# Kernel optimization log

Hardware: AMD Instinct MI355X
Metric: run time of the kernel (lower is better)

## Reference

```python
import jax, jax.numpy as jnp
import numpy as np

D_MODEL = 128
NHEAD = 8
NLAYERS = 6
LAYER_NAMES = ['self', 'cross', 'self', 'cross', 'self', 'cross']
TEMPERATURE = 5.0
EPS = 1e-6


def _pos_encoding(x):
    # Sinusoidal 1D position encoding along the width axis. x: [N, H, W, C]
    C, W = x.shape[-1], x.shape[2]
    pos = jnp.arange(W, dtype=x.dtype)[:, None]                      # [W,1]
    div = jnp.exp(jnp.arange(0, C, 2, dtype=x.dtype) * (-np.log(10000.0) / C))
    pe = jnp.zeros((W, C), x.dtype)
    pe = pe.at[:, 0::2].set(jnp.sin(pos * div))
    pe = pe.at[:, 1::2].set(jnp.cos(pos * div))
    return x + pe[None, None]                                        # broadcast over N,H


def _linear_attention(q, k, v):
    # q,k,v: [N, H, W, nhead, dim]; kernelized linear attention along W
    Q = jax.nn.elu(q) + 1.0
    K = jax.nn.elu(k) + 1.0
    v_len = v.shape[2]
    V = v / v_len
    KV = jnp.einsum('nhsed,nhsev->nhedv', K, V)                      # [N,H,e,d,d]
    Z = 1.0 / (jnp.einsum('nhled,nhed->nhle', Q, K.sum(axis=2)) + EPS)
    return jnp.einsum('nhled,nhedv,nhle->nhlev', Q, KV, Z) * v_len


def _layer_norm(x, g, b):
    m = x.mean(-1, keepdims=True)
    v = jnp.mean((x - m) ** 2, -1, keepdims=True)
    return (x - m) / jnp.sqrt(v + 1e-5) * g + b


def _encoder_layer(x, source, Wq, Wk, Wv, Wm, W1, W2, g1, b1, g2, b2):
    x = _pos_encoding(x)
    source = _pos_encoding(source)
    bs, h, w, c = x.shape
    e, d = NHEAD, c // NHEAD
    q = (x @ Wq).reshape(bs, h, w, e, d)
    k = (source @ Wk).reshape(bs, h, w, e, d)
    v = (source @ Wv).reshape(bs, h, w, e, d)
    msg = _linear_attention(q, k, v).reshape(bs, h, w, c) @ Wm
    msg = _layer_norm(msg, g1, b1)
    msg = jnp.concatenate([x, msg], axis=-1)                         # [N,H,W,2C]
    msg = jax.nn.relu(msg @ W1) @ W2
    msg = _layer_norm(msg, g2, b2)
    return x + msg


def _forward(feat0, feat1, Wq, Wk, Wv, Wm, W1, W2, g1, b1, g2, b2):
    feat0 = feat0.transpose(0, 2, 3, 1)                              # [N,H,W,C]
    feat1 = feat1.transpose(0, 2, 3, 1)
    for i, name in enumerate(LAYER_NAMES):
        p = (Wq[i], Wk[i], Wv[i], Wm[i], W1[i], W2[i], g1[i], b1[i], g2[i], b2[i])
        if name == 'self':
            feat0 = _encoder_layer(feat0, feat0, *p)
            feat1 = _encoder_layer(feat1, feat1, *p)
        else:  # cross: sequential update (feat1 sees updated feat0), as in torch source
            feat0 = _encoder_layer(feat0, feat1, *p)
            feat1 = _encoder_layer(feat1, feat0, *p)
    w = feat0.shape[2]
    attn_mask = jnp.where(jnp.triu(jnp.ones((w, w), bool), 1), -jnp.inf, 0.0)
    attn_mask = attn_mask[None, None].astype(feat0.dtype)
    scale = feat0.shape[-1] ** 0.5
    sim = jnp.einsum('ntwc,ntlc->ntwl', feat0 / scale, feat1 / scale) / TEMPERATURE
    return sim + attn_mask


def setup_inputs() -> dict:
    key = jax.random.key(0)
    ks = jax.random.split(key, 12)
    N, C, H, W = 2, D_MODEL, 64, 640
    L, D = NLAYERS, D_MODEL
    s = 1.0 / np.sqrt(D)
    s2 = 1.0 / np.sqrt(2 * D)
    return {
        'feat0': jax.random.normal(ks[0], (N, C, H, W), jnp.float32),
        'feat1': jax.random.normal(ks[1], (N, C, H, W), jnp.float32),
        'Wq': jax.random.normal(ks[2], (L, D, D), jnp.float32) * s,
        'Wk': jax.random.normal(ks[3], (L, D, D), jnp.float32) * s,
        'Wv': jax.random.normal(ks[4], (L, D, D), jnp.float32) * s,
        'Wm': jax.random.normal(ks[5], (L, D, D), jnp.float32) * s,
        'W1': jax.random.normal(ks[6], (L, 2 * D, 2 * D), jnp.float32) * s2,
        'W2': jax.random.normal(ks[7], (L, 2 * D, D), jnp.float32) * s2,
        'g1': jnp.ones((L, D), jnp.float32),
        'b1': jnp.zeros((L, D), jnp.float32),
        'g2': jnp.ones((L, D), jnp.float32),
        'b2': jnp.zeros((L, D), jnp.float32),
    }


def reference(feat0, feat1, Wq, Wk, Wv, Wm, W1, W2, g1, b1, g2, b2):
    return _forward(feat0, feat1, Wq, Wk, Wv, Wm, W1, W2, g1, b1, g2, b2)
```

## Files before the change

### kernel.cpp

```cpp
#include <hip/hip_runtime.h>
#include <cmath>
#include <math.h>

#define TOK 81920
#define WDIM 640

typedef __attribute__((ext_vector_type(8))) short short8v;
typedef __attribute__((ext_vector_type(4))) short short4v;
typedef __attribute__((ext_vector_type(4))) float f32x4;

__device__ __forceinline__ short f2bf(float f) {
  __bf16 h = (__bf16)f;
  short s;
  __builtin_memcpy(&s, &h, 2);
  return s;
}
__device__ __forceinline__ float bf2f(short s) {
  union { unsigned u; float f; } x; x.u = ((unsigned)(unsigned short)s) << 16;
  return x.f;
}

__global__ __launch_bounds__(256) void pe_kernel(float* __restrict__ pe) {
  int id = blockIdx.x * 256 + threadIdx.x;
  if (id >= WDIM * 128) return;
  int w = id >> 7;
  int c = id & 127;
  float i2 = (float)(c & 126);
  float freq = expf(i2 * -0.071955784156063941f);
  float ang = (float)w * freq;
  pe[id] = (c & 1) ? cosf(ang) : sinf(ang);
}

__global__ __launch_bounds__(256) void tr_kernel(const float* __restrict__ in0,
                                                 const float* __restrict__ in1,
                                                 short* __restrict__ x0,
                                                 short* __restrict__ x1) {
  __shared__ float t[32][33];
  int w0 = blockIdx.x * 32;
  int c0 = blockIdx.y * 32;
  int z = blockIdx.z;
  int feat = z >> 7;
  int nh = z & 127;
  int n = nh >> 6, h = nh & 63;
  const float* in = feat ? in1 : in0;
  short* out = feat ? x1 : x0;
  int tx = threadIdx.x & 31, ty = threadIdx.x >> 5;
  const float* ip = in + ((n * 128 + c0) * 64 + h) * 640 + w0;
#pragma unroll
  for (int i = 0; i < 32; i += 8)
    t[ty + i][tx] = ip[(ty + i) * (64 * 640) + tx];
  __syncthreads();
  short* op = out + ((size_t)(n * 64 + h) * 640 + w0) * 128 + c0;
#pragma unroll
  for (int i = 0; i < 32; i += 8)
    op[(size_t)(ty + i) * 128 + tx] = f2bf(t[tx][ty + i]);
}

__global__ __launch_bounds__(256) void wprep_kernel(
    const float* __restrict__ Wq, const float* __restrict__ Wk,
    const float* __restrict__ Wv, const float* __restrict__ Wm,
    const float* __restrict__ W1, const float* __restrict__ W2,
    short* __restrict__ BT) {
  int id = blockIdx.x * 256 + threadIdx.x;
  if (id >= 6 * 163840) return;
  int layer = id / 163840;
  int r = id % 163840;
  float v;
  if (r < 65536) {
    int seg = r >> 14;
    int rr = r & 16383;
    int n = rr >> 7, k = rr & 127;
    const float* W = seg == 0 ? Wq : seg == 1 ? Wk : seg == 2 ? Wv : Wm;
    v = W[layer * 16384 + k * 128 + n];
  } else if (r < 131072) {
    int rr = r - 65536;
    int n = rr >> 8, k = rr & 255;
    v = W1[layer * 65536 + k * 256 + n];
  } else {
    int rr = r - 131072;
    int n = rr >> 8, k = rr & 255;
    v = W2[layer * 32768 + k * 128 + n];
  }
  BT[id] = f2bf(v);
}

__device__ __forceinline__ void load_af(const short* __restrict__ A,
                                        const float* __restrict__ pe,
                                        int bm, int wr, int l15, int lk,
                                        short8v af[4][4]) {
  const int wbase = bm % WDIM;
#pragma unroll
  for (int mf = 0; mf < 4; ++mf) {
    const int rl = wr * 64 + mf * 16 + l15;
    const short* ar = A + (size_t)(bm + rl) * 128;
    const float* pr = pe + (size_t)(wbase + rl) * 128;
#pragma unroll
    for (int ks = 0; ks < 4; ++ks) {
      const int kloc = ks * 32 + lk * 8;
      short8v xa = *(const short8v*)(ar + kloc);
      f32x4 p0 = *(const f32x4*)(pr + kloc);
      f32x4 p1 = *(const f32x4*)(pr + kloc + 4);
      short8v o;
      o[0] = f2bf(bf2f(xa[0]) + p0[0]); o[1] = f2bf(bf2f(xa[1]) + p0[1]);
      o[2] = f2bf(bf2f(xa[2]) + p0[2]); o[3] = f2bf(bf2f(xa[3]) + p0[3]);
      o[4] = f2bf(bf2f(xa[4]) + p1[0]); o[5] = f2bf(bf2f(xa[5]) + p1[1]);
      o[6] = f2bf(bf2f(xa[6]) + p1[2]); o[7] = f2bf(bf2f(xa[7]) + p1[3]);
      af[ks][mf] = o;
    }
  }
}

__device__ __forceinline__ void proj_pass_T(const short8v af[4][4],
                                            const short* __restrict__ WT,
                                            int wr, int wc, int l15, int lk,
                                            short (*tS)[136]) {
  f32x4 acc[4][4] = {};
#pragma unroll
  for (int ks = 0; ks < 4; ++ks) {
    const int kloc = ks * 32 + lk * 8;
    short8v bfr[4];
#pragma unroll
    for (int nf = 0; nf < 4; ++nf)
      bfr[nf] = *(const short8v*)&WT[(size_t)(wc * 64 + nf * 16 + l15) * 128 + kloc];
#pragma unroll
    for (int mf = 0; mf < 4; ++mf)
#pragma unroll
      for (int nf = 0; nf < 4; ++nf)
        acc[mf][nf] = __builtin_amdgcn_mfma_f32_16x16x32_bf16(
            bfr[nf], af[ks][mf], acc[mf][nf], 0, 0, 0);
  }
#pragma unroll
  for (int mf = 0; mf < 4; ++mf)
#pragma unroll
    for (int nf = 0; nf < 4; ++nf) {
      short4v p;
      p[0] = f2bf(acc[mf][nf][0]); p[1] = f2bf(acc[mf][nf][1]);
      p[2] = f2bf(acc[mf][nf][2]); p[3] = f2bf(acc[mf][nf][3]);
      *(short4v*)&tS[wr * 64 + mf * 16 + l15][wc * 64 + nf * 16 + lk * 4] = p;
    }
}

__device__ __forceinline__ void tile_out(const short (*tS)[136], int bm, int tid,
                                         short* __restrict__ out) {
#pragma unroll
  for (int it = 0; it < 8; ++it) {
    int u = it * 256 + tid;
    int row = u >> 4, seg = u & 15;
    *(short8v*)&out[(size_t)(bm + row) * 128 + seg * 8] =
        *(const short8v*)&tS[row][seg * 8];
  }
}

__global__ __launch_bounds__(256) void qkv_self_kernel(
    const short* __restrict__ x0, const short* __restrict__ x1,
    const float* __restrict__ pe,
    const short* __restrict__ wqT, const short* __restrict__ wkT,
    const short* __restrict__ wvT,
    short* q0, short* k0, short* v0, short* q1, short* k1, short* v1) {
  __shared__ short tS[128][136];
  const int tid = threadIdx.x, lane = tid & 63, wid = tid >> 6;
  const int wr = wid >> 1, wc = wid & 1;
  const int bm = blockIdx.x * 128;
  const int l15 = lane & 15, lk = lane >> 4;
  const int z = blockIdx.z;
  const short* A = z ? x1 : x0;
  short8v af[4][4];
  load_af(A, pe, bm, wr, l15, lk, af);
  proj_pass_T(af, wqT, wr, wc, l15, lk, tS);
  __syncthreads();
  tile_out(tS, bm, tid, z ? q1 : q0);
  __syncthreads();
  proj_pass_T(af, wkT, wr, wc, l15, lk, tS);
  __syncthreads();
  tile_out(tS, bm, tid, z ? k1 : k0);
  __syncthreads();
  proj_pass_T(af, wvT, wr, wc, l15, lk, tS);
  __syncthreads();
  tile_out(tS, bm, tid, z ? v1 : v0);
}

__global__ __launch_bounds__(256) void qkv_cross_kernel(
    const short* __restrict__ xq, const short* __restrict__ xs,
    const float* __restrict__ pe,
    const short* __restrict__ wqT, const short* __restrict__ wkT,
    const short* __restrict__ wvT,
    short* qb, short* kb, short* vb) {
  __shared__ short tS[128][136];
  const int tid = threadIdx.x, lane = tid & 63, wid = tid >> 6;
  const int wr = wid >> 1, wc = wid & 1;
  const int bm = blockIdx.x * 128;
  const int l15 = lane & 15, lk = lane >> 4;
  short8v af[4][4];
  if (blockIdx.y == 0) {
    load_af(xq, pe, bm, wr, l15, lk, af);
    proj_pass_T(af, wqT, wr, wc, l15, lk, tS);
    __syncthreads();
    tile_out(tS, bm, tid, qb);
  } else {
    load_af(xs, pe, bm, wr, l15, lk, af);
    proj_pass_T(af, wkT, wr, wc, l15, lk, tS);
    __syncthreads();
    tile_out(tS, bm, tid, kb);
    __syncthreads();
    proj_pass_T(af, wvT, wr, wc, l15, lk, tS);
    __syncthreads();
    tile_out(tS, bm, tid, vb);
  }
}

template <int NSC>
__global__ __launch_bounds__(256) void kv_kernel(
    const short* __restrict__ k0, const short* __restrict__ v0,
    const short* __restrict__ k1, const short* __restrict__ v1,
    float* __restrict__ kvp) {
  const int bid = blockIdx.x;
  const int sc = bid % NSC;
  const int e = bid / NSC;
  const int strip = sc / 5, chunk = sc % 5;
  const short* kb = (strip >= 128) ? k1 : k0;
  const short* vb = (strip >= 128) ? v1 : v0;
  const int nh = strip & 127;
  const size_t base = (size_t)nh * (640 * 128) + (size_t)chunk * (128 * 128) + e * 16;
  __shared__ float Ks[128][16];
  __shared__ float Vs[128][16];
  const int tid = threadIdx.x;
  const int srow = tid >> 1, shalf = (tid & 1) * 8;
  short8v k8 = *(const short8v*)&kb[base + (size_t)srow * 128 + shalf];
  short8v v8 = *(const short8v*)&vb[base + (size_t)srow * 128 + shalf];
#pragma unroll
  for (int j = 0; j < 8; ++j) {
    float kr = bf2f(k8[j]);
    Ks[srow][shalf + j] = kr > 0.f ? kr + 1.f : __expf(kr);
    Vs[srow][shalf + j] = bf2f(v8[j]);
  }
  __syncthreads();
  const int d = tid >> 4, vv = tid & 15;
  float kv = 0.f, ks = 0.f;
#pragma unroll 8
  for (int sl = 0; sl < 128; ++sl) {
    float kk = Ks[sl][d];
    kv = fmaf(kk, Vs[sl][vv], kv);
    ks += kk;
  }
  float* out = kvp + ((size_t)(strip * 8 + e) * 5 + chunk) * 272;
  out[d * 16 + vv] = kv;
  if (vv == 0) out[256 + d] = ks;
}

template <int DUAL>
__global__ __launch_bounds__(256) void apply_wm_kernel(
    short* q0, short* q1, const float* __restrict__ kvp,
    const short* __restrict__ wmT,
    const float* __restrict__ g, const float* __restrict__ b) {
  const int bid = blockIdx.x;
  const int strip = bid / 10, lc = bid % 10;
  __shared__ float KV8[8][16][17];
  __shared__ float KS8[8][16];
  __shared__ short oS[64][136];
  const int tid = threadIdx.x;
  for (int idx = tid; idx < 8 * 272; idx += 256) {
    int e = idx / 272, r = idx - e * 272;
    const float* p = kvp + ((size_t)(strip * 8 + e) * 5) * 272 + r;
    float s = ((p[0] + p[272]) + (p[544] + p[816])) + p[1088];
    if (r < 256) KV8[e][r >> 4][r & 15] = s;
    else         KS8[e][r - 256] = s;
  }
  __syncthreads();
  short* qb = (DUAL && strip >= 128) ? q1 : q0;
  const int nh = strip & 127;
  const int lrow = tid >> 2;
  const int row = lc * 64 + lrow;
  const int cb = (tid & 3) * 32;
  short* qp = qb + (size_t)nh * (640 * 128) + (size_t)row * 128 + cb;
  short8v qv0 = *(const short8v*)(qp);
  short8v qv1 = *(const short8v*)(qp + 8);
  short8v qv2 = *(const short8v*)(qp + 16);
  short8v qv3 = *(const short8v*)(qp + 24);
  float qe[32];
#pragma unroll
  for (int j = 0; j < 8; ++j) {
    float a = bf2f(qv0[j]); qe[j]      = a > 0.f ? a + 1.f : __expf(a);
    float c1 = bf2f(qv1[j]); qe[8 + j]  = c1 > 0.f ? c1 + 1.f : __expf(c1);
    float c2 = bf2f(qv2[j]); qe[16 + j] = c2 > 0.f ? c2 + 1.f : __expf(c2);
    float c3 = bf2f(qv3[j]); qe[24 + j] = c3 > 0.f ? c3 + 1.f : __expf(c3);
  }
  short res[32];
#pragma unroll
  for (int h = 0; h < 2; ++h) {
    const int e = (cb >> 4) + h;
    const float* Q = qe + h * 16;
    float dz = 0.f;
#pragma unroll
    for (int dd = 0; dd < 16; ++dd) dz = fmaf(Q[dd], KS8[e][dd], dz);
    const float zi = 1.f / (dz + 1e-6f);
#pragma unroll
    for (int vv = 0; vv < 16; ++vv) {
      float o = 0.f;
#pragma unroll
      for (int dd = 0; dd < 16; ++dd) o = fmaf(Q[dd], KV8[e][dd][vv], o);
      res[h * 16 + vv] = f2bf(o * zi);
    }
  }
  short8v w0, w1, w2, w3;
#pragma unroll
  for (int j = 0; j < 8; ++j) {
    w0[j] = res[j]; w1[j] = res[8 + j]; w2[j] = res[16 + j]; w3[j] = res[24 + j];
  }
  *(short8v*)&oS[lrow][cb]      = w0;
  *(short8v*)&oS[lrow][cb + 8]  = w1;
  *(short8v*)&oS[lrow][cb + 16] = w2;
  *(short8v*)&oS[lrow][cb + 24] = w3;
  __syncthreads();
  const int lane = tid & 63, wv = tid >> 6;
  const int l15 = lane & 15, lk = lane >> 4;
  f32x4 acc[8] = {};
#pragma unroll
  for (int ks = 0; ks < 4; ++ks) {
    const int kloc = ks * 32 + lk * 8;
    short8v afr = *(const short8v*)&oS[wv * 16 + l15][kloc];
    short8v bfr[8];
#pragma unroll
    for (int nf = 0; nf < 8; ++nf)
      bfr[nf] = *(const short8v*)&wmT[(size_t)(nf * 16 + l15) * 128 + kloc];
#pragma unroll
    for (int nf = 0; nf < 8; ++nf)
      acc[nf] = __builtin_amdgcn_mfma_f32_16x16x32_bf16(bfr[nf], afr, acc[nf], 0, 0, 0);
  }
  float s = 0.f, qq = 0.f;
#pragma unroll
  for (int nf = 0; nf < 8; ++nf)
#pragma unroll
    for (int r = 0; r < 4; ++r) {
      s += acc[nf][r];
      qq = fmaf(acc[nf][r], acc[nf][r], qq);
    }
  s += __shfl_xor(s, 16);  qq += __shfl_xor(qq, 16);
  s += __shfl_xor(s, 32);  qq += __shfl_xor(qq, 32);
  float mean = s * (1.f / 128.f);
  float var = qq * (1.f / 128.f) - mean * mean;
  float rstd = rsqrtf(var + 1e-5f);
#pragma unroll
  for (int nf = 0; nf < 8; ++nf) {
    f32x4 g4 = *(const f32x4*)&g[nf * 16 + lk * 4];
    f32x4 b4 = *(const f32x4*)&b[nf * 16 + lk * 4];
    short4v p;
#pragma unroll
    for (int r = 0; r < 4; ++r)
      p[r] = f2bf((acc[nf][r] - mean) * rstd * g4[r] + b4[r]);
    *(short4v*)&oS[wv * 16 + l15][nf * 16 + lk * 4] = p;
  }
  __syncthreads();
  short* mp = qb + (size_t)nh * (640 * 128) + (size_t)(lc * 64) * 128;
#pragma unroll
  for (int it = 0; it < 4; ++it) {
    int u = it * 256 + tid;
    int rw = u >> 4, seg = u & 15;
    *(short8v*)&mp[(size_t)rw * 128 + seg * 8] = *(const short8v*)&oS[rw][seg * 8];
  }
}

__global__ __launch_bounds__(256) void w1_kernel(
    const short* __restrict__ xA, const short* __restrict__ xB,
    const short* __restrict__ mA, const short* __restrict__ mB,
    const float* __restrict__ pe, const short* __restrict__ w1T,
    short* h0A, short* h1A, short* h0B, short* h1B) {
  __shared__ short tS[128][136];
  const int z = blockIdx.z;
  const short* x = z ? xB : xA;
  const short* m = z ? mB : mA;
  short* h0 = z ? h0B : h0A;
  short* h1 = z ? h1B : h1A;
  const int tid = threadIdx.x, lane = tid & 63, wid = tid >> 6;
  const int wr = wid >> 1, wc = wid & 1;
  const int bm = blockIdx.x * 128;
  const int l15 = lane & 15, lk = lane >> 4;
  const int wbase = bm % WDIM;
  for (int p = 0; p < 2; ++p) {
    f32x4 acc[4][4] = {};
#pragma unroll
    for (int ks = 0; ks < 8; ++ks) {
      const int kloc = ks * 32 + lk * 8;
      short8v bfr[4], afr[4];
#pragma unroll
      for (int nf = 0; nf < 4; ++nf)
        bfr[nf] = *(const short8v*)&w1T[(size_t)(p * 128 + wc * 64 + nf * 16 + l15) * 256 + kloc];
      if (ks < 4) {
#pragma unroll
        for (int mf = 0; mf < 4; ++mf) {
          const int rl = wr * 64 + mf * 16 + l15;
          short8v xa = *(const short8v*)(x + (size_t)(bm + rl) * 128 + kloc);
          const float* pr = pe + (size_t)(wbase + rl) * 128 + kloc;
          f32x4 p0 = *(const f32x4*)pr;
          f32x4 p1 = *(const f32x4*)(pr + 4);
          short8v ov;
          ov[0] = f2bf(bf2f(xa[0]) + p0[0]); ov[1] = f2bf(bf2f(xa[1]) + p0[1]);
          ov[2] = f2bf(bf2f(xa[2]) + p0[2]); ov[3] = f2bf(bf2f(xa[3]) + p0[3]);
          ov[4] = f2bf(bf2f(xa[4]) + p1[0]); ov[5] = f2bf(bf2f(xa[5]) + p1[1]);
          ov[6] = f2bf(bf2f(xa[6]) + p1[2]); ov[7] = f2bf(bf2f(xa[7]) + p1[3]);
          afr[mf] = ov;
        }
      } else {
#pragma unroll
        for (int mf = 0; mf < 4; ++mf)
          afr[mf] = *(const short8v*)&m[(size_t)(bm + wr * 64 + mf * 16 + l15) * 128 + kloc - 128];
      }
#pragma unroll
      for (int mf = 0; mf < 4; ++mf)
#pragma unroll
        for (int nf = 0; nf < 4; ++nf)
          acc[mf][nf] = __builtin_amdgcn_mfma_f32_16x16x32_bf16(
              bfr[nf], afr[mf], acc[mf][nf], 0, 0, 0);
    }
#pragma unroll
    for (int mf = 0; mf < 4; ++mf)
#pragma unroll
      for (int nf = 0; nf < 4; ++nf) {
        short4v pk;
#pragma unroll
        for (int r = 0; r < 4; ++r)
          pk[r] = f2bf(fmaxf(acc[mf][nf][r], 0.f));
        *(short4v*)&tS[wr * 64 + mf * 16 + l15][wc * 64 + nf * 16 + lk * 4] = pk;
      }
    __syncthreads();
    tile_out(tS, bm, tid, p ? h1 : h0);
    __syncthreads();
  }
}

__global__ __launch_bounds__(256) void w2_ln_kernel(
    const short* __restrict__ h0A, const short* __restrict__ h1A,
    const short* __restrict__ h0B, const short* __restrict__ h1B,
    const short* __restrict__ w2T, short* xA, short* xB,
    const float* __restrict__ pe, const float* __restrict__ g,
    const float* __restrict__ b) {
  __shared__ short tS[128][136];
  __shared__ float lds_s[2][128];
  __shared__ float lds_q[2][128];
  const int z = blockIdx.z;
  const short* h0 = z ? h0B : h0A;
  const short* h1 = z ? h1B : h1A;
  short* x = z ? xB : xA;
  const int tid = threadIdx.x, lane = tid & 63, wid = tid >> 6;
  const int wr = wid >> 1, wc = wid & 1;
  const int bm = blockIdx.x * 128;
  const int l15 = lane & 15, lk = lane >> 4;
  const int wbase = bm % WDIM;
  f32x4 acc[4][4] = {};
#pragma unroll
  for (int ks = 0; ks < 8; ++ks) {
    const int kloc = ks * 32 + lk * 8;
    const short* hp = (ks < 4) ? h0 : h1;
    const int kl = (ks < 4) ? kloc : kloc - 128;
    short8v bfr[4], afr[4];
#pragma unroll
    for (int nf = 0; nf < 4; ++nf)
      bfr[nf] = *(const short8v*)&w2T[(size_t)(wc * 64 + nf * 16 + l15) * 256 + kloc];
#pragma unroll
    for (int mf = 0; mf < 4; ++mf)
      afr[mf] = *(const short8v*)&hp[(size_t)(bm + wr * 64 + mf * 16 + l15) * 128 + kl];
#pragma unroll
    for (int mf = 0; mf < 4; ++mf)
#pragma unroll
      for (int nf = 0; nf < 4; ++nf)
        acc[mf][nf] = __builtin_amdgcn_mfma_f32_16x16x32_bf16(
            bfr[nf], afr[mf], acc[mf][nf], 0, 0, 0);
  }
#pragma unroll
  for (int mf = 0; mf < 4; ++mf) {
    float s = 0.f, qq = 0.f;
#pragma unroll
    for (int nf = 0; nf < 4; ++nf)
#pragma unroll
      for (int r = 0; r < 4; ++r) {
        s += acc[mf][nf][r];
        qq = fmaf(acc[mf][nf][r], acc[mf][nf][r], qq);
      }
    s += __shfl_xor(s, 16);  qq += __shfl_xor(qq, 16);
    s += __shfl_xor(s, 32);  qq += __shfl_xor(qq, 32);
    if (lk == 0) {
      int rl = wr * 64 + mf * 16 + l15;
      lds_s[wc][rl] = s;
      lds_q[wc][rl] = qq;
    }
  }
  __syncthreads();
#pragma unroll
  for (int mf = 0; mf < 4; ++mf) {
    int rl = wr * 64 + mf * 16 + l15;
    float mean = (lds_s[0][rl] + lds_s[1][rl]) * (1.f / 128.f);
    float var = (lds_q[0][rl] + lds_q[1][rl]) * (1.f / 128.f) - mean * mean;
    float rstd = rsqrtf(var + 1e-5f);
#pragma unroll
    for (int nf = 0; nf < 4; ++nf) {
      f32x4 g4 = *(const f32x4*)&g[wc * 64 + nf * 16 + lk * 4];
      f32x4 b4 = *(const f32x4*)&b[wc * 64 + nf * 16 + lk * 4];
      short4v pk;
#pragma unroll
      for (int r = 0; r < 4; ++r)
        pk[r] = f2bf((acc[mf][nf][r] - mean) * rstd * g4[r] + b4[r]);
      *(short4v*)&tS[rl][wc * 64 + nf * 16 + lk * 4] = pk;
    }
  }
  __syncthreads();
#pragma unroll
  for (int it = 0; it < 8; ++it) {
    int u = it * 256 + tid;
    int row = u >> 4, seg = u & 15;
    size_t xi = (size_t)(bm + row) * 128 + seg * 8;
    short8v xv8 = *(const short8v*)&x[xi];
    short8v t8 = *(const short8v*)&tS[row][seg * 8];
    const float* pr = pe + (size_t)(wbase + row) * 128 + seg * 8;
    f32x4 p0 = *(const f32x4*)pr;
    f32x4 p1 = *(const f32x4*)(pr + 4);
    short8v o8;
    o8[0] = f2bf(bf2f(xv8[0]) + p0[0] + bf2f(t8[0]));
    o8[1] = f2bf(bf2f(xv8[1]) + p0[1] + bf2f(t8[1]));
    o8[2] = f2bf(bf2f(xv8[2]) + p0[2] + bf2f(t8[2]));
    o8[3] = f2bf(bf2f(xv8[3]) + p0[3] + bf2f(t8[3]));
    o8[4] = f2bf(bf2f(xv8[4]) + p1[0] + bf2f(t8[4]));
    o8[5] = f2bf(bf2f(xv8[5]) + p1[1] + bf2f(t8[5]));
    o8[6] = f2bf(bf2f(xv8[6]) + p1[2] + bf2f(t8[6]));
    o8[7] = f2bf(bf2f(xv8[7]) + p1[3] + bf2f(t8[7]));
    *(short8v*)&x[xi] = o8;
  }
}

__global__ __launch_bounds__(256) void sim_mfma(const short* __restrict__ f0,
                                                const short* __restrict__ f1,
                                                float* __restrict__ out) {
  const int fid = (blockIdx.z * 5 + blockIdx.y) * 5 + blockIdx.x;
  const int c8 = fid & 7, kk_ = fid >> 3;
  const int nt = c8 * 16 + kk_ / 25;
  const int r2 = kk_ % 25;
  const int bw = (r2 % 5) * 128;
  const int bl = (r2 / 5) * 128;
  const int tid = threadIdx.x;
  if (bl > bw) {
    f32x4 m4 = {-1e30f, -1e30f, -1e30f, -1e30f};
#pragma unroll
    for (int it = 0; it < 16; ++it) {
      int u = it * 256 + tid;
      int row = u >> 5, c4 = u & 31;
      *(f32x4*)&out[((size_t)nt * 640 + bw + row) * 640 + bl + c4 * 4] = m4;
    }
    return;
  }
  const int lane = tid & 63;
  const int wid = tid >> 6;
  const int wr = wid >> 1, wc = wid & 1;
  const short* __restrict__ A = f0 + (size_t)nt * 640 * 128;
  const short* __restrict__ B = f1 + (size_t)nt * 640 * 128;
  const int l15 = lane & 15;
  const int lk = lane >> 4;
  f32x4 acc[4][4] = {};
#pragma unroll
  for (int ks = 0; ks < 4; ++ks) {
    const int kloc = ks * 32 + lk * 8;
    short8v afr[4], bfr[4];
#pragma unroll
    for (int mf = 0; mf < 4; ++mf)
      afr[mf] = *(const short8v*)&A[(size_t)(bw + wr * 64 + mf * 16 + l15) * 128 + kloc];
#pragma unroll
    for (int nf = 0; nf < 4; ++nf)
      bfr[nf] = *(const short8v*)&B[(size_t)(bl + wc * 64 + nf * 16 + l15) * 128 + kloc];
#pragma unroll
    for (int mf = 0; mf < 4; ++mf)
#pragma unroll
      for (int nf = 0; nf < 4; ++nf)
        acc[mf][nf] = __builtin_amdgcn_mfma_f32_16x16x32_bf16(
            afr[mf], bfr[nf], acc[mf][nf], 0, 0, 0);
  }
#pragma unroll
  for (int mf = 0; mf < 4; ++mf)
#pragma unroll
    for (int nf = 0; nf < 4; ++nf) {
      const int l = bl + wc * 64 + nf * 16 + l15;
#pragma unroll
      for (int r = 0; r < 4; ++r) {
        const int w = bw + wr * 64 + mf * 16 + lk * 4 + r;
        float v = acc[mf][nf][r] * (1.f / 640.f);
        if (l > w) v = -1e30f;
        out[((size_t)nt * 640 + w) * 640 + l] = v;
      }
    }
}

extern "C" void kernel_launch(void* const* d_in, const int* in_sizes, int n_in,
                              void* d_out, int out_size, void* d_ws, size_t ws_size,
                              hipStream_t stream) {
  (void)in_sizes; (void)n_in; (void)out_size; (void)ws_size;
  const float* feat0 = (const float*)d_in[0];
  const float* feat1 = (const float*)d_in[1];
  const float* Wq = (const float*)d_in[2];
  const float* Wk = (const float*)d_in[3];
  const float* Wv = (const float*)d_in[4];
  const float* Wm = (const float*)d_in[5];
  const float* W1 = (const float*)d_in[6];
  const float* W2 = (const float*)d_in[7];
  const float* g1 = (const float*)d_in[8];
  const float* b1 = (const float*)d_in[9];
  const float* g2 = (const float*)d_in[10];
  const float* b2 = (const float*)d_in[11];

  float* wsf = (float*)d_ws;
  const size_t U = (size_t)TOK * 128;
  float* pe = wsf;
  short* x0 = (short*)(wsf + 81920);
  short* x1 = x0 + U;
  short* q0 = x1 + U;
  short* k0 = q0 + U;
  short* v0 = k0 + U;
  short* q1 = v0 + U;
  short* k1 = q1 + U;
  short* v1 = k1 + U;
  short* bt = v1 + U;
  float* kvp = (float*)(bt + 983040);

  dim3 blk(256);
  pe_kernel<<<dim3(320), blk, 0, stream>>>(pe);
  tr_kernel<<<dim3(20, 4, 256), blk, 0, stream>>>(feat0, feat1, x0, x1);
  wprep_kernel<<<dim3((6 * 163840 + 255) / 256), blk, 0, stream>>>(
      Wq, Wk, Wv, Wm, W1, W2, bt);

  const int NB = TOK / 128;
  for (int i = 0; i < 6; ++i) {
    const short* bt_i = bt + (size_t)i * 163840;
    const short* wqT = bt_i;
    const short* wkT = bt_i + 16384;
    const short* wvT = bt_i + 32768;
    const short* wmT = bt_i + 49152;
    const short* w1T = bt_i + 65536;
    const short* w2T = bt_i + 131072;
    const float* g1_i = g1 + i * 128;
    const float* b1_i = b1 + i * 128;
    const float* g2_i = g2 + i * 128;
    const float* b2_i = b2 + i * 128;
    if ((i & 1) == 0) {
      qkv_self_kernel<<<dim3(NB, 1, 2), blk, 0, stream>>>(
          x0, x1, pe, wqT, wkT, wvT, q0, k0, v0, q1, k1, v1);
      kv_kernel<1280><<<dim3(8 * 1280), blk, 0, stream>>>(k0, v0, k1, v1, kvp);
      apply_wm_kernel<1><<<dim3(2560), blk, 0, stream>>>(q0, q1, kvp, wmT, g1_i, b1_i);
      w1_kernel<<<dim3(NB, 1, 2), blk, 0, stream>>>(
          x0, x1, q0, q1, pe, w1T, k0, v0, k1, v1);
      w2_ln_kernel<<<dim3(NB, 1, 2), blk, 0, stream>>>(
          k0, v0, k1, v1, w2T, x0, x1, pe, g2_i, b2_i);
    } else {
      qkv_cross_kernel<<<dim3(NB, 2), blk, 0, stream>>>(
          x0, x1, pe, wqT, wkT, wvT, q0, k0, v0);
      kv_kernel<640><<<dim3(8 * 640), blk, 0, stream>>>(k0, v0, k0, v0, kvp);
      apply_wm_kernel<0><<<dim3(1280), blk, 0, stream>>>(q0, q0, kvp, wmT, g1_i, b1_i);
      w1_kernel<<<dim3(NB, 1, 1), blk, 0, stream>>>(
          x0, x0, q0, q0, pe, w1T, k0, v0, k0, v0);
      w2_ln_kernel<<<dim3(NB, 1, 1), blk, 0, stream>>>(
          k0, v0, k0, v0, w2T, x0, x0, pe, g2_i, b2_i);

      qkv_cross_kernel<<<dim3(NB, 2), blk, 0, stream>>>(
          x1, x0, pe, wqT, wkT, wvT, q0, k0, v0);
      kv_kernel<640><<<dim3(8 * 640), blk, 0, stream>>>(k0, v0, k0, v0, kvp);
      apply_wm_kernel<0><<<dim3(1280), blk, 0, stream>>>(q0, q0, kvp, wmT, g1_i, b1_i);
      w1_kernel<<<dim3(NB, 1, 1), blk, 0, stream>>>(
          x1, x1, q0, q0, pe, w1T, k0, v0, k0, v0);
      w2_ln_kernel<<<dim3(NB, 1, 1), blk, 0, stream>>>(
          k0, v0, k0, v0, w2T, x1, x1, pe, g2_i, b2_i);
    }
  }
  sim_mfma<<<dim3(5, 5, 128), blk, 0, stream>>>(x0, x1, (float*)d_out);
}
```

Baseline: 2.381 ms.

## Shrink projection and FFN GEMM tiles to 64 rows with 4 column-split waves

The QKV, W1 and W2+LayerNorm kernels now process 64-row tiles instead of 128, with each of the four waves covering all 64 rows and a 32-column slice rather than a 2x2 wave grid. This doubles the block count and halves accumulator registers and shared memory, aiming at better occupancy and load balance across CUs. The LayerNorm row reduction now combines four wave partials, and the LDS row pitch changes to 140. In exchange, each wave repeats the activation loads and the positional-encoding add, so per-block reuse of A fragments goes down.

```diff
diff --git a/kernel.cpp b/kernel.cpp
--- a/kernel.cpp
+++ b/kernel.cpp
@@ -84,14 +84,15 @@
   BT[id] = f2bf(v);
 }
 
-__device__ __forceinline__ void load_af(const short* __restrict__ A,
-                                        const float* __restrict__ pe,
-                                        int bm, int wr, int l15, int lk,
-                                        short8v af[4][4]) {
+
+__device__ __forceinline__ void load_af64(const short* __restrict__ A,
+                                          const float* __restrict__ pe,
+                                          int bm, int l15, int lk,
+                                          short8v af[4][4]) {
   const int wbase = bm % WDIM;
 #pragma unroll
   for (int mf = 0; mf < 4; ++mf) {
-    const int rl = wr * 64 + mf * 16 + l15;
+    const int rl = mf * 16 + l15;
     const short* ar = A + (size_t)(bm + rl) * 128;
     const float* pr = pe + (size_t)(wbase + rl) * 128;
 #pragma unroll
@@ -110,40 +111,40 @@
   }
 }
 
-__device__ __forceinline__ void proj_pass_T(const short8v af[4][4],
+__device__ __forceinline__ void proj_pass64(const short8v af[4][4],
                                             const short* __restrict__ WT,
-                                            int wr, int wc, int l15, int lk,
-                                            short (*tS)[136]) {
-  f32x4 acc[4][4] = {};
+                                            int wq, int l15, int lk,
+                                            short (*tS)[140]) {
+  f32x4 acc[4][2] = {};
 #pragma unroll
   for (int ks = 0; ks < 4; ++ks) {
     const int kloc = ks * 32 + lk * 8;
-    short8v bfr[4];
-#pragma unroll
-    for (int nf = 0; nf < 4; ++nf)
-      bfr[nf] = *(const short8v*)&WT[(size_t)(wc * 64 + nf * 16 + l15) * 128 + kloc];
+    short8v bfr[2];
+#pragma unroll
+    for (int nf = 0; nf < 2; ++nf)
+      bfr[nf] = *(const short8v*)&WT[(size_t)(wq * 32 + nf * 16 + l15) * 128 + kloc];
 #pragma unroll
     for (int mf = 0; mf < 4; ++mf)
 #pragma unroll
-      for (int nf = 0; nf < 4; ++nf)
+      for (int nf = 0; nf < 2; ++nf)
         acc[mf][nf] = __builtin_amdgcn_mfma_f32_16x16x32_bf16(
             bfr[nf], af[ks][mf], acc[mf][nf], 0, 0, 0);
   }
 #pragma unroll
   for (int mf = 0; mf < 4; ++mf)
 #pragma unroll
-    for (int nf = 0; nf < 4; ++nf) {
+    for (int nf = 0; nf < 2; ++nf) {
       short4v p;
       p[0] = f2bf(acc[mf][nf][0]); p[1] = f2bf(acc[mf][nf][1]);
       p[2] = f2bf(acc[mf][nf][2]); p[3] = f2bf(acc[mf][nf][3]);
-      *(short4v*)&tS[wr * 64 + mf * 16 + l15][wc * 64 + nf * 16 + lk * 4] = p;
-    }
-}
-
-__device__ __forceinline__ void tile_out(const short (*tS)[136], int bm, int tid,
-                                         short* __restrict__ out) {
-#pragma unroll
-  for (int it = 0; it < 8; ++it) {
+      *(short4v*)&tS[mf * 16 + l15][wq * 32 + nf * 16 + lk * 4] = p;
+    }
+}
+
+__device__ __forceinline__ void tile_out64(const short (*tS)[140], int bm, int tid,
+                                           short* __restrict__ out) {
+#pragma unroll
+  for (int it = 0; it < 4; ++it) {
     int u = it * 256 + tid;
     int row = u >> 4, seg = u & 15;
     *(short8v*)&out[(size_t)(bm + row) * 128 + seg * 8] =
@@ -157,26 +158,25 @@
     const short* __restrict__ wqT, const short* __restrict__ wkT,
     const short* __restrict__ wvT,
     short* q0, short* k0, short* v0, short* q1, short* k1, short* v1) {
-  __shared__ short tS[128][136];
-  const int tid = threadIdx.x, lane = tid & 63, wid = tid >> 6;
-  const int wr = wid >> 1, wc = wid & 1;
-  const int bm = blockIdx.x * 128;
+  __shared__ short tS[64][140];
+  const int tid = threadIdx.x, lane = tid & 63, wq = tid >> 6;
+  const int bm = blockIdx.x * 64;
   const int l15 = lane & 15, lk = lane >> 4;
   const int z = blockIdx.z;
   const short* A = z ? x1 : x0;
   short8v af[4][4];
-  load_af(A, pe, bm, wr, l15, lk, af);
-  proj_pass_T(af, wqT, wr, wc, l15, lk, tS);
-  __syncthreads();
-  tile_out(tS, bm, tid, z ? q1 : q0);
-  __syncthreads();
-  proj_pass_T(af, wkT, wr, wc, l15, lk, tS);
-  __syncthreads();
-  tile_out(tS, bm, tid, z ? k1 : k0);
-  __syncthreads();
-  proj_pass_T(af, wvT, wr, wc, l15, lk, tS);
-  __syncthreads();
-  tile_out(tS, bm, tid, z ? v1 : v0);
+  load_af64(A, pe, bm, l15, lk, af);
+  proj_pass64(af, wqT, wq, l15, lk, tS);
+  __syncthreads();
+  tile_out64(tS, bm, tid, z ? q1 : q0);
+  __syncthreads();
+  proj_pass64(af, wkT, wq, l15, lk, tS);
+  __syncthreads();
+  tile_out64(tS, bm, tid, z ? k1 : k0);
+  __syncthreads();
+  proj_pass64(af, wvT, wq, l15, lk, tS);
+  __syncthreads();
+  tile_out64(tS, bm, tid, z ? v1 : v0);
 }
 
 __global__ __launch_bounds__(256) void qkv_cross_kernel(
@@ -185,26 +185,25 @@
     const short* __restrict__ wqT, const short* __restrict__ wkT,
     const short* __restrict__ wvT,
     short* qb, short* kb, short* vb) {
-  __shared__ short tS[128][136];
-  const int tid = threadIdx.x, lane = tid & 63, wid = tid >> 6;
-  const int wr = wid >> 1, wc = wid & 1;
-  const int bm = blockIdx.x * 128;
+  __shared__ short tS[64][140];
+  const int tid = threadIdx.x, lane = tid & 63, wq = tid >> 6;
+  const int bm = blockIdx.x * 64;
   const int l15 = lane & 15, lk = lane >> 4;
   short8v af[4][4];
   if (blockIdx.y == 0) {
-    load_af(xq, pe, bm, wr, l15, lk, af);
-    proj_pass_T(af, wqT, wr, wc, l15, lk, tS);
+    load_af64(xq, pe, bm, l15, lk, af);
+    proj_pass64(af, wqT, wq, l15, lk, tS);
     __syncthreads();
-    tile_out(tS, bm, tid, qb);
+    tile_out64(tS, bm, tid, qb);
   } else {
-    load_af(xs, pe, bm, wr, l15, lk, af);
-    proj_pass_T(af, wkT, wr, wc, l15, lk, tS);
+    load_af64(xs, pe, bm, l15, lk, af);
+    proj_pass64(af, wkT, wq, l15, lk, tS);
     __syncthreads();
-    tile_out(tS, bm, tid, kb);
+    tile_out64(tS, bm, tid, kb);
     __syncthreads();
-    proj_pass_T(af, wvT, wr, wc, l15, lk, tS);
+    proj_pass64(af, wvT, wq, l15, lk, tS);
     __syncthreads();
-    tile_out(tS, bm, tid, vb);
+    tile_out64(tS, bm, tid, vb);
   }
 }
 
@@ -364,30 +363,29 @@
     const short* __restrict__ mA, const short* __restrict__ mB,
     const float* __restrict__ pe, const short* __restrict__ w1T,
     short* h0A, short* h1A, short* h0B, short* h1B) {
-  __shared__ short tS[128][136];
+  __shared__ short tS[64][140];
   const int z = blockIdx.z;
   const short* x = z ? xB : xA;
   const short* m = z ? mB : mA;
   short* h0 = z ? h0B : h0A;
   short* h1 = z ? h1B : h1A;
-  const int tid = threadIdx.x, lane = tid & 63, wid = tid >> 6;
-  const int wr = wid >> 1, wc = wid & 1;
-  const int bm = blockIdx.x * 128;
+  const int tid = threadIdx.x, lane = tid & 63, wq = tid >> 6;
+  const int bm = blockIdx.x * 64;
   const int l15 = lane & 15, lk = lane >> 4;
   const int wbase = bm % WDIM;
   for (int p = 0; p < 2; ++p) {
-    f32x4 acc[4][4] = {};
+    f32x4 acc[4][2] = {};
 #pragma unroll
     for (int ks = 0; ks < 8; ++ks) {
       const int kloc = ks * 32 + lk * 8;
-      short8v bfr[4], afr[4];
-#pragma unroll
-      for (int nf = 0; nf < 4; ++nf)
-        bfr[nf] = *(const short8v*)&w1T[(size_t)(p * 128 + wc * 64 + nf * 16 + l15) * 256 + kloc];
+      short8v bfr[2], afr[4];
+#pragma unroll
+      for (int nf = 0; nf < 2; ++nf)
+        bfr[nf] = *(const short8v*)&w1T[(size_t)(p * 128 + wq * 32 + nf * 16 + l15) * 256 + kloc];
       if (ks < 4) {
 #pragma unroll
         for (int mf = 0; mf < 4; ++mf) {
-          const int rl = wr * 64 + mf * 16 + l15;
+          const int rl = mf * 16 + l15;
           short8v xa = *(const short8v*)(x + (size_t)(bm + rl) * 128 + kloc);
           const float* pr = pe + (size_t)(wbase + rl) * 128 + kloc;
           f32x4 p0 = *(const f32x4*)pr;
@@ -402,27 +400,27 @@
       } else {
 #pragma unroll
         for (int mf = 0; mf < 4; ++mf)
-          afr[mf] = *(const short8v*)&m[(size_t)(bm + wr * 64 + mf * 16 + l15) * 128 + kloc - 128];
+          afr[mf] = *(const short8v*)&m[(size_t)(bm + mf * 16 + l15) * 128 + kloc - 128];
       }
 #pragma unroll
       for (int mf = 0; mf < 4; ++mf)
 #pragma unroll
-        for (int nf = 0; nf < 4; ++nf)
+        for (int nf = 0; nf < 2; ++nf)
           acc[mf][nf] = __builtin_amdgcn_mfma_f32_16x16x32_bf16(
               bfr[nf], afr[mf], acc[mf][nf], 0, 0, 0);
     }
 #pragma unroll
     for (int mf = 0; mf < 4; ++mf)
 #pragma unroll
-      for (int nf = 0; nf < 4; ++nf) {
+      for (int nf = 0; nf < 2; ++nf) {
         short4v pk;
 #pragma unroll
         for (int r = 0; r < 4; ++r)
           pk[r] = f2bf(fmaxf(acc[mf][nf][r], 0.f));
-        *(short4v*)&tS[wr * 64 + mf * 16 + l15][wc * 64 + nf * 16 + lk * 4] = pk;
+        *(short4v*)&tS[mf * 16 + l15][wq * 32 + nf * 16 + lk * 4] = pk;
       }
     __syncthreads();
-    tile_out(tS, bm, tid, p ? h1 : h0);
+    tile_out64(tS, bm, tid, p ? h1 : h0);
     __syncthreads();
   }
 }
@@ -433,35 +431,34 @@
     const short* __restrict__ w2T, short* xA, short* xB,
     const float* __restrict__ pe, const float* __restrict__ g,
     const float* __restrict__ b) {
-  __shared__ short tS[128][136];
-  __shared__ float lds_s[2][128];
-  __shared__ float lds_q[2][128];
+  __shared__ short tS[64][140];
+  __shared__ float lds_s[4][64];
+  __shared__ float lds_q[4][64];
   const int z = blockIdx.z;
   const short* h0 = z ? h0B : h0A;
   const short* h1 = z ? h1B : h1A;
   short* x = z ? xB : xA;
-  const int tid = threadIdx.x, lane = tid & 63, wid = tid >> 6;
-  const int wr = wid >> 1, wc = wid & 1;
-  const int bm = blockIdx.x * 128;
+  const int tid = threadIdx.x, lane = tid & 63, wq = tid >> 6;
+  const int bm = blockIdx.x * 64;
   const int l15 = lane & 15, lk = lane >> 4;
   const int wbase = bm % WDIM;
-  f32x4 acc[4][4] = {};
+  f32x4 acc[4][2] = {};
 #pragma unroll
   for (int ks = 0; ks < 8; ++ks) {
     const int kloc = ks * 32 + lk * 8;
     const short* hp = (ks < 4) ? h0 : h1;
     const int kl = (ks < 4) ? kloc : kloc - 128;
-    short8v bfr[4], afr[4];
-#pragma unroll
-    for (int nf = 0; nf < 4; ++nf)
-      bfr[nf] = *(const short8v*)&w2T[(size_t)(wc * 64 + nf * 16 + l15) * 256 + kloc];
+    short8v bfr[2], afr[4];
+#pragma unroll
+    for (int nf = 0; nf < 2; ++nf)
+      bfr[nf] = *(const short8v*)&w2T[(size_t)(wq * 32 + nf * 16 + l15) * 256 + kloc];
 #pragma unroll
     for (int mf = 0; mf < 4; ++mf)
-      afr[mf] = *(const short8v*)&hp[(size_t)(bm + wr * 64 + mf * 16 + l15) * 128 + kl];
+      afr[mf] = *(const short8v*)&hp[(size_t)(bm + mf * 16 + l15) * 128 + kl];
 #pragma unroll
     for (int mf = 0; mf < 4; ++mf)
 #pragma unroll
-      for (int nf = 0; nf < 4; ++nf)
+      for (int nf = 0; nf < 2; ++nf)
         acc[mf][nf] = __builtin_amdgcn_mfma_f32_16x16x32_bf16(
             bfr[nf], afr[mf], acc[mf][nf], 0, 0, 0);
   }
@@ -469,7 +466,7 @@
   for (int mf = 0; mf < 4; ++mf) {
     float s = 0.f, qq = 0.f;
 #pragma unroll
-    for (int nf = 0; nf < 4; ++nf)
+    for (int nf = 0; nf < 2; ++nf)
 #pragma unroll
       for (int r = 0; r < 4; ++r) {
         s += acc[mf][nf][r];
@@ -478,32 +475,34 @@
     s += __shfl_xor(s, 16);  qq += __shfl_xor(qq, 16);
     s += __shfl_xor(s, 32);  qq += __shfl_xor(qq, 32);
     if (lk == 0) {
-      int rl = wr * 64 + mf * 16 + l15;
-      lds_s[wc][rl] = s;
-      lds_q[wc][rl] = qq;
+      int rl = mf * 16 + l15;
+      lds_s[wq][rl] = s;
+      lds_q[wq][rl] = qq;
     }
   }
   __syncthreads();
 #pragma unroll
   for (int mf = 0; mf < 4; ++mf) {
-    int rl = wr * 64 + mf * 16 + l15;
-    float mean = (lds_s[0][rl] + lds_s[1][rl]) * (1.f / 128.f);
-    float var = (lds_q[0][rl] + lds_q[1][rl]) * (1.f / 128.f) - mean * mean;
+    int rl = mf * 16 + l15;
+    float ssum = (lds_s[0][rl] + lds_s[1][rl]) + (lds_s[2][rl] + lds_s[3][rl]);
+    float qsum = (lds_q[0][rl] + lds_q[1][rl]) + (lds_q[2][rl] + lds_q[3][rl]);
+    float mean = ssum * (1.f / 128.f);
+    float var = qsum * (1.f / 128.f) - mean * mean;
     float rstd = rsqrtf(var + 1e-5f);
 #pragma unroll
-    for (int nf = 0; nf < 4; ++nf) {
-      f32x4 g4 = *(const f32x4*)&g[wc * 64 + nf * 16 + lk * 4];
-      f32x4 b4 = *(const f32x4*)&b[wc * 64 + nf * 16 + lk * 4];
+    for (int nf = 0; nf < 2; ++nf) {
+      f32x4 g4 = *(const f32x4*)&g[wq * 32 + nf * 16 + lk * 4];
+      f32x4 b4 = *(const f32x4*)&b[wq * 32 + nf * 16 + lk * 4];
       short4v pk;
 #pragma unroll
       for (int r = 0; r < 4; ++r)
         pk[r] = f2bf((acc[mf][nf][r] - mean) * rstd * g4[r] + b4[r]);
-      *(short4v*)&tS[rl][wc * 64 + nf * 16 + lk * 4] = pk;
-    }
-  }
-  __syncthreads();
-#pragma unroll
-  for (int it = 0; it < 8; ++it) {
+      *(short4v*)&tS[rl][wq * 32 + nf * 16 + lk * 4] = pk;
+    }
+  }
+  __syncthreads();
+#pragma unroll
+  for (int it = 0; it < 4; ++it) {
     int u = it * 256 + tid;
     int row = u >> 4, seg = u & 15;
     size_t xi = (size_t)(bm + row) * 128 + seg * 8;
@@ -622,7 +621,7 @@
   wprep_kernel<<<dim3((6 * 163840 + 255) / 256), blk, 0, stream>>>(
       Wq, Wk, Wv, Wm, W1, W2, bt);
 
-  const int NB = TOK / 128;
+  const int NB64 = TOK / 64;
   for (int i = 0; i < 6; ++i) {
     const short* bt_i = bt + (size_t)i * 163840;
     const short* wqT = bt_i;
@@ -636,31 +635,31 @@
     const float* g2_i = g2 + i * 128;
     const float* b2_i = b2 + i * 128;
     if ((i & 1) == 0) {
-      qkv_self_kernel<<<dim3(NB, 1, 2), blk, 0, stream>>>(
+      qkv_self_kernel<<<dim3(NB64, 1, 2), blk, 0, stream>>>(
           x0, x1, pe, wqT, wkT, wvT, q0, k0, v0, q1, k1, v1);
       kv_kernel<1280><<<dim3(8 * 1280), blk, 0, stream>>>(k0, v0, k1, v1, kvp);
       apply_wm_kernel<1><<<dim3(2560), blk, 0, stream>>>(q0, q1, kvp, wmT, g1_i, b1_i);
-      w1_kernel<<<dim3(NB, 1, 2), blk, 0, stream>>>(
+      w1_kernel<<<dim3(NB64, 1, 2), blk, 0, stream>>>(
           x0, x1, q0, q1, pe, w1T, k0, v0, k1, v1);
-      w2_ln_kernel<<<dim3(NB, 1, 2), blk, 0, stream>>>(
+      w2_ln_kernel<<<dim3(NB64, 1, 2), blk, 0, stream>>>(
           k0, v0, k1, v1, w2T, x0, x1, pe, g2_i, b2_i);
     } else {
-      qkv_cross_kernel<<<dim3(NB, 2), blk, 0, stream>>>(
+      qkv_cross_kernel<<<dim3(NB64, 2), blk, 0, stream>>>(
           x0, x1, pe, wqT, wkT, wvT, q0, k0, v0);
       kv_kernel<640><<<dim3(8 * 640), blk, 0, stream>>>(k0, v0, k0, v0, kvp);
       apply_wm_kernel<0><<<dim3(1280), blk, 0, stream>>>(q0, q0, kvp, wmT, g1_i, b1_i);
-      w1_kernel<<<dim3(NB, 1, 1), blk, 0, stream>>>(
+      w1_kernel<<<dim3(NB64, 1, 1), blk, 0, stream>>>(
           x0, x0, q0, q0, pe, w1T, k0, v0, k0, v0);
-      w2_ln_kernel<<<dim3(NB, 1, 1), blk, 0, stream>>>(
+      w2_ln_kernel<<<dim3(NB64, 1, 1), blk, 0, stream>>>(
           k0, v0, k0, v0, w2T, x0, x0, pe, g2_i, b2_i);
 
-      qkv_cross_kernel<<<dim3(NB, 2), blk, 0, stream>>>(
+      qkv_cross_kernel<<<dim3(NB64, 2), blk, 0, stream>>>(
           x1, x0, pe, wqT, wkT, wvT, q0, k0, v0);
       kv_kernel<640><<<dim3(8 * 640), blk, 0, stream>>>(k0, v0, k0, v0, kvp);
       apply_wm_kernel<0><<<dim3(1280), blk, 0, stream>>>(q0, q0, kvp, wmT, g1_i, b1_i);
-      w1_kernel<<<dim3(NB, 1, 1), blk, 0, stream>>>(
+      w1_kernel<<<dim3(NB64, 1, 1), blk, 0, stream>>>(
           x1, x1, q0, q0, pe, w1T, k0, v0, k0, v0);
-      w2_ln_kernel<<<dim3(NB, 1, 1), blk, 0, stream>>>(
+      w2_ln_kernel<<<dim3(NB64, 1, 1), blk, 0, stream>>>(
           k0, v0, k0, v0, w2T, x1, x1, pe, g2_i, b2_i);
     }
   }
```

Measured after the change: 2.735 ms. +14.9%, slower.
